# Kernel optimization log

Measured on AMD Instinct MI355X. Metric: run time of the kernel, lower is better.

The kernel has to match this reference:

```python
import jax, jax.numpy as jnp
import numpy as np

# bi-degrees (0,0),(1,0),(0,1),(1,1) -> d = (2a+1)*(2b+1)
DEG_DIMS = [1, 3, 3, 9]
P, C = 8192, 256


def setup_inputs() -> dict:
    key = jax.random.key(0)
    kx, k0, k1, k2 = jax.random.split(key, 4)
    scale = 1.0 / np.sqrt(C).astype(np.float32)
    x = jax.random.normal(kx, (P, C, sum(DEG_DIMS)), dtype=jnp.float32)
    # torch.randn(mo, mi) / sqrt(mi); W10 is shared by degrees (1,0) and (0,1)
    W00 = jax.random.normal(k0, (C, C), dtype=jnp.float32) * scale
    W10 = jax.random.normal(k1, (C, C), dtype=jnp.float32) * scale
    W11 = jax.random.normal(k2, (C, C), dtype=jnp.float32) * scale
    return {"x": x, "W00": W00, "W10": W10, "W11": W11}


def reference(x, W00, W10, W11):
    # Weight for each degree segment; (0,1) reuses W10 (parameter tying in GLinear)
    Ws = [W00, W10, W10, W11]
    offsets = np.concatenate([[0], np.cumsum(DEG_DIMS)])
    outs = []
    for W, a, b in zip(Ws, offsets[:-1], offsets[1:]):
        v = x[:, :, a:b]                      # (p, c_in, d_k)
        outs.append(jnp.einsum('oi,pid->pod', W, v))
    out = jnp.concatenate(outs, axis=-1)      # (p, c_out, sum_d)
    # use_skip with matching shared channel -> residual add of input
    return out + x
```

## Files before the change

kernel.cpp:

```cpp
#include <hip/hip_runtime.h>
#include <hip/hip_bf16.h>


#define C_DIM   256
#define D_DIM   16
#define P_TILE  16
#define KC      64
#define LDS_ROW 72
#define UNITS   4
#define NFRAG   (2 * 8 * 24 * 64)
#define WS_NEEDED (NFRAG * 16)

typedef __attribute__((ext_vector_type(8))) short  short8v;
typedef __attribute__((ext_vector_type(4))) float  float4v;
typedef __attribute__((ext_vector_type(4))) unsigned int uint4v;

__device__ __forceinline__ unsigned int pack_bf16x2_rne(float lo, float hi) {
    unsigned int ul = __builtin_bit_cast(unsigned int, lo);
    unsigned int uh = __builtin_bit_cast(unsigned int, hi);
    ul = (ul + 0x7fffu + ((ul >> 16) & 1u)) >> 16;
    uh = (uh + 0x7fffu + ((uh >> 16) & 1u));
    return (ul & 0xffffu) | (uh & 0xffff0000u);
}

__device__ __forceinline__ unsigned int pack_bf16x2_tr(float lo, float hi) {
    return __builtin_amdgcn_perm(__builtin_bit_cast(unsigned int, hi),
                                 __builtin_bit_cast(unsigned int, lo),
                                 0x07060302u);
}

__device__ __forceinline__ short8v load_w_frag(const float* __restrict__ W, int row, int col) {
    const float* p = W + (size_t)row * C_DIM + col;
    float4v a = *(const float4v*)p;
    float4v b = *(const float4v*)(p + 4);
    uint4v u;
    u.x = pack_bf16x2_tr(a.x, a.y);
    u.y = pack_bf16x2_tr(a.z, a.w);
    u.z = pack_bf16x2_tr(b.x, b.y);
    u.w = pack_bf16x2_tr(b.z, b.w);
    return __builtin_bit_cast(short8v, u);
}

__device__ __forceinline__ void glds16(const float* g, float* l) {
    __builtin_amdgcn_global_load_lds(
        (const __attribute__((address_space(1))) void*)g,
        (__attribute__((address_space(3))) void*)l,
        16, 0, 0);
}

__global__ __launch_bounds__(256, 4) void init_w_pack(
    const float* __restrict__ W00, const float* __restrict__ W10,
    const float* __restrict__ W11, uint4v* __restrict__ ws)
{
    const int tid = blockIdx.x * 256 + threadIdx.x;
    if (tid >= NFRAG) return;
    const int l   = tid & 63;
    int idx = tid >> 6;
    const int f  = idx % 24;
    idx /= 24;
    const int w  = idx & 7;
    const int oh = idx >> 3;
    const int mat = f % 3;
    const int ks  = (f / 3) & 1;
    const int ic  = f / 6;
    const float* Wm = (mat == 0) ? W00 : (mat == 1) ? W10 : W11;
    const int row = oh * 128 + w * 16 + (l & 15);
    const int col = ic * KC + ks * 32 + (l >> 4) * 8;
    const float* p = Wm + (size_t)row * C_DIM + col;
    float4v a = *(const float4v*)p;
    float4v b = *(const float4v*)(p + 4);
    uint4v u;
    u.x = pack_bf16x2_rne(a.x, a.y);
    u.y = pack_bf16x2_rne(a.z, a.w);
    u.z = pack_bf16x2_rne(b.x, b.y);
    u.w = pack_bf16x2_rne(b.z, b.w);
    ws[tid] = u;
}

__global__ __launch_bounds__(512, 2) void glinear_kernel(
    const float* __restrict__ x, const float* __restrict__ W00,
    const float* __restrict__ W10, const float* __restrict__ W11,
    float* __restrict__ out, const short8v* __restrict__ wpack, int use_ws)
{
    __shared__ __align__(16) float f32s[64 * 256];
    __shared__ __align__(16) unsigned short ls[2][P_TILE * D_DIM * LDS_ROW];

    const int t    = threadIdx.x;
    const int lane = t & 63;
    const int w    = t >> 6;
    const int lm   = lane & 15;
    const int quad = lane >> 4;

    const int oh    = blockIdx.x & 1;
    const int pg    = blockIdx.x >> 1;
    const int obase = oh * 128 + w * 16;
    const int orow  = obase + lm;

    const int d4    = t & 3;
    const int ip    = (t >> 2) & 31;
    const int pq    = t >> 7;
    const int i_loc = ip * 2;

    short8v wf[4][2][3];
    if (use_ws && wpack != nullptr) {
        const short8v* wbase = wpack + ((size_t)(oh * 8 + w) * 24) * 64 + lane;
        #pragma unroll
        for (int ic = 0; ic < 4; ++ic)
            #pragma unroll
            for (int ks = 0; ks < 2; ++ks)
                #pragma unroll
                for (int mat = 0; mat < 3; ++mat)
                    wf[ic][ks][mat] = wbase[(size_t)(ic * 6 + ks * 3 + mat) * 64];
    } else {
        #pragma unroll
        for (int ic = 0; ic < 4; ++ic)
            #pragma unroll
            for (int ks = 0; ks < 2; ++ks) {
                const int col = ic * KC + ks * 32 + quad * 8;
                wf[ic][ks][0] = load_w_frag(W00, orow, col);
                wf[ic][ks][1] = load_w_frag(W10, orow, col);
                wf[ic][ks][2] = load_w_frag(W11, orow, col);
            }
    }
    asm volatile("" ::: "memory");

    auto stage_chunk = [&](int pb, int ic) {
        #pragma unroll
        for (int it = 0; it < 4; ++it) {
            const float* src = x + ((size_t)(pb + pq + it * 4) * C_DIM
                                    + (ic * KC + i_loc)) * D_DIM + d4 * 4;
            glds16(src,         &f32s[((it * 2 + 0) * 8 + w) << 8]);
            glds16(src + D_DIM, &f32s[((it * 2 + 1) * 8 + w) << 8]);
        }
    };

    stage_chunk(pg * UNITS * P_TILE, 0);

    for (int u = 0; u < UNITS; ++u) {
        const int pbase = (pg * UNITS + u) * P_TILE;

        float4v acc[16];
        const float4v fzero = {0.f, 0.f, 0.f, 0.f};
        #pragma unroll
        for (int b = 0; b < 16; ++b) acc[b] = fzero;

        #pragma unroll
        for (int ic = 0; ic < 4; ++ic) {
            const int ib = ic & 1;

            asm volatile("s_waitcnt vmcnt(0)" ::: "memory");

            #pragma unroll
            for (int it = 0; it < 4; ++it) {
                const int p = pq + it * 4;
                float4v a = *(const float4v*)&f32s[((((it * 2 + 0) * 8 + w) << 8)) + lane * 4];
                float4v b = *(const float4v*)&f32s[((((it * 2 + 1) * 8 + w) << 8)) + lane * 4];
                const int g = (i_loc >> 3) ^ (p & 7);
                const int e = i_loc & 7;
                const int base = (p * D_DIM + d4 * 4) * LDS_ROW + g * 8 + e;
                #pragma unroll
                for (int dj = 0; dj < 4; ++dj) {
                    *(unsigned int*)(&ls[ib][base + dj * LDS_ROW]) = pack_bf16x2_rne(a[dj], b[dj]);
                }
            }
            __syncthreads();

            if (ic < 3)               stage_chunk(pbase, ic + 1);
            else if (u < UNITS - 1)   stage_chunk(pbase + P_TILE, 0);
            asm volatile("" ::: "memory");

            #pragma unroll
            for (int ks = 0; ks < 2; ++ks) {
                const int gq = ((ks * 4 + quad) ^ (lm & 7));
                const unsigned short* brow = &ls[ib][lm * D_DIM * LDS_ROW + gq * 8];

                #pragma unroll
                for (int dd = 0; dd < 16; ++dd) {
                    short8v xf = *(const short8v*)(brow + dd * LDS_ROW);
                    short8v wv = (dd == 0) ? wf[ic][ks][0]
                               : (dd <= 6) ? wf[ic][ks][1]
                                           : wf[ic][ks][2];
                    acc[dd] = __builtin_amdgcn_mfma_f32_16x16x32_bf16(xf, wv, acc[dd], 0, 0, 0);
                }
            }
        }

        #pragma unroll
        for (int r = 0; r < 4; ++r) {
            const int p = pbase + quad * 4 + r;
            const int o = obase + lm;
            const size_t off = (size_t)p * (C_DIM * D_DIM) + (size_t)o * D_DIM;
            #pragma unroll
            for (int g = 0; g < 4; ++g) {
                float4v v;
                v.x = acc[g * 4 + 0][r];
                v.y = acc[g * 4 + 1][r];
                v.z = acc[g * 4 + 2][r];
                v.w = acc[g * 4 + 3][r];
                float4v xr = *(const float4v*)(x + off + g * 4);
                *(float4v*)(out + off + g * 4) = v + xr;
            }
        }
    }
}

extern "C" void kernel_launch(void* const* d_in, const int* in_sizes, int n_in,
                              void* d_out, int out_size, void* d_ws, size_t ws_size,
                              hipStream_t stream) {
    const float* x   = (const float*)d_in[0];
    const float* W00 = (const float*)d_in[1];
    const float* W10 = (const float*)d_in[2];
    const float* W11 = (const float*)d_in[3];
    float* out = (float*)d_out;

    const int use_ws = (d_ws != nullptr && ws_size >= WS_NEEDED) ? 1 : 0;
    if (use_ws) {
        hipLaunchKernelGGL(init_w_pack, dim3(96), dim3(256), 0, stream,
                           W00, W10, W11, (uint4v*)d_ws);
    }
    hipLaunchKernelGGL(glinear_kernel, dim3(256), dim3(512), 0, stream,
                       x, W00, W10, W11, out, (const short8v*)d_ws, use_ws);
}
```

Before: 279.5 us.

## Halve K-chunk and stream weight fragments per chunk to double occupancy

The input-channel chunk drops from 64 to 32, so the fp32 staging and bf16 LDS buffers shrink. Weight fragments are no longer all held in registers up front; each chunk's fragments are loaded just before that chunk is used. Together these cut LDS and VGPR use enough to raise launch bounds to 4 blocks per CU, and the grid grows to 512 blocks with 2 units each. The trade-off is twice as many barriers and staging rounds per tile, plus weight loads from global/L2 inside the main loop instead of once per block.

```diff
diff --git a/kernel.cpp b/kernel.cpp
--- a/kernel.cpp
+++ b/kernel.cpp
@@ -5,9 +5,10 @@
 #define C_DIM   256
 #define D_DIM   16
 #define P_TILE  16
-#define KC      64
-#define LDS_ROW 72
-#define UNITS   4
+#define KC      32
+#define NCH     8
+#define LDS_ROW 40
+#define UNITS   2
 #define NFRAG   (2 * 8 * 24 * 64)
 #define WS_NEEDED (NFRAG * 16)
 
@@ -65,7 +66,7 @@
     const int ic  = f / 6;
     const float* Wm = (mat == 0) ? W00 : (mat == 1) ? W10 : W11;
     const int row = oh * 128 + w * 16 + (l & 15);
-    const int col = ic * KC + ks * 32 + (l >> 4) * 8;
+    const int col = ic * 64 + ks * 32 + (l >> 4) * 8;
     const float* p = Wm + (size_t)row * C_DIM + col;
     float4v a = *(const float4v*)p;
     float4v b = *(const float4v*)(p + 4);
@@ -77,63 +78,54 @@
     ws[tid] = u;
 }
 
-__global__ __launch_bounds__(512, 2) void glinear_kernel(
+__global__ __launch_bounds__(512, 4) void glinear_kernel(
     const float* __restrict__ x, const float* __restrict__ W00,
     const float* __restrict__ W10, const float* __restrict__ W11,
     float* __restrict__ out, const short8v* __restrict__ wpack, int use_ws)
 {
-    __shared__ __align__(16) float f32s[64 * 256];
-    __shared__ __align__(16) unsigned short ls[2][P_TILE * D_DIM * LDS_ROW];
+    __shared__ __align__(16) float f32s[32 * 256];
+    __shared__ __align__(16) unsigned short ls[2][256 * LDS_ROW];
 
     const int t    = threadIdx.x;
     const int lane = t & 63;
     const int w    = t >> 6;
     const int lm   = lane & 15;
     const int quad = lane >> 4;
+    const int d4   = lane & 3;
+    const int ip   = (lane >> 2) & 15;
 
     const int oh    = blockIdx.x & 1;
     const int pg    = blockIdx.x >> 1;
     const int obase = oh * 128 + w * 16;
     const int orow  = obase + lm;
 
-    const int d4    = t & 3;
-    const int ip    = (t >> 2) & 31;
-    const int pq    = t >> 7;
-    const int i_loc = ip * 2;
-
-    short8v wf[4][2][3];
-    if (use_ws && wpack != nullptr) {
-        const short8v* wbase = wpack + ((size_t)(oh * 8 + w) * 24) * 64 + lane;
-        #pragma unroll
-        for (int ic = 0; ic < 4; ++ic)
-            #pragma unroll
-            for (int ks = 0; ks < 2; ++ks)
-                #pragma unroll
-                for (int mat = 0; mat < 3; ++mat)
-                    wf[ic][ks][mat] = wbase[(size_t)(ic * 6 + ks * 3 + mat) * 64];
-    } else {
-        #pragma unroll
-        for (int ic = 0; ic < 4; ++ic)
-            #pragma unroll
-            for (int ks = 0; ks < 2; ++ks) {
-                const int col = ic * KC + ks * 32 + quad * 8;
-                wf[ic][ks][0] = load_w_frag(W00, orow, col);
-                wf[ic][ks][1] = load_w_frag(W10, orow, col);
-                wf[ic][ks][2] = load_w_frag(W11, orow, col);
-            }
-    }
-    asm volatile("" ::: "memory");
-
-    auto stage_chunk = [&](int pb, int ic) {
-        #pragma unroll
-        for (int it = 0; it < 4; ++it) {
-            const float* src = x + ((size_t)(pb + pq + it * 4) * C_DIM
-                                    + (ic * KC + i_loc)) * D_DIM + d4 * 4;
-            glds16(src,         &f32s[((it * 2 + 0) * 8 + w) << 8]);
-            glds16(src + D_DIM, &f32s[((it * 2 + 1) * 8 + w) << 8]);
+    const short8v* wbase = wpack + ((size_t)(oh * 8 + w) * 24) * 64 + lane;
+
+    short8v wf[NCH][3];
+    auto loadW = [&](int c) {
+        if (use_ws) {
+            #pragma unroll
+            for (int mat = 0; mat < 3; ++mat)
+                wf[c][mat] = wbase[(size_t)((c >> 1) * 6 + (c & 1) * 3 + mat) * 64];
+        } else {
+            const int col = (c >> 1) * 64 + (c & 1) * 32 + quad * 8;
+            wf[c][0] = load_w_frag(W00, orow, col);
+            wf[c][1] = load_w_frag(W10, orow, col);
+            wf[c][2] = load_w_frag(W11, orow, col);
         }
     };
 
+    auto stage_chunk = [&](int pb, int c) {
+        #pragma unroll
+        for (int j = 0; j < 4; ++j) {
+            const int p = w + (j >> 1) * 8;
+            const int i = c * KC + ip * 2 + (j & 1);
+            const float* src = x + ((size_t)(pb + p) * C_DIM + i) * D_DIM + d4 * 4;
+            glds16(src, &f32s[(w * 4 + j) << 8]);
+        }
+    };
+
+    loadW(0);
     stage_chunk(pg * UNITS * P_TILE, 0);
 
     for (int u = 0; u < UNITS; ++u) {
@@ -145,43 +137,40 @@
         for (int b = 0; b < 16; ++b) acc[b] = fzero;
 
         #pragma unroll
-        for (int ic = 0; ic < 4; ++ic) {
-            const int ib = ic & 1;
+        for (int c = 0; c < NCH; ++c) {
+            const int ib = c & 1;
 
             asm volatile("s_waitcnt vmcnt(0)" ::: "memory");
 
             #pragma unroll
-            for (int it = 0; it < 4; ++it) {
-                const int p = pq + it * 4;
-                float4v a = *(const float4v*)&f32s[((((it * 2 + 0) * 8 + w) << 8)) + lane * 4];
-                float4v b = *(const float4v*)&f32s[((((it * 2 + 1) * 8 + w) << 8)) + lane * 4];
-                const int g = (i_loc >> 3) ^ (p & 7);
-                const int e = i_loc & 7;
-                const int base = (p * D_DIM + d4 * 4) * LDS_ROW + g * 8 + e;
+            for (int m = 0; m < 2; ++m) {
+                const int p = w + m * 8;
+                float4v a = *(const float4v*)&f32s[((w * 4 + m * 2 + 0) << 8) + lane * 4];
+                float4v b = *(const float4v*)&f32s[((w * 4 + m * 2 + 1) << 8) + lane * 4];
+                const int cb = (((ip >> 2) ^ (p & 3)) * 8 + (ip & 3) * 2);
                 #pragma unroll
                 for (int dj = 0; dj < 4; ++dj) {
-                    *(unsigned int*)(&ls[ib][base + dj * LDS_ROW]) = pack_bf16x2_rne(a[dj], b[dj]);
+                    const int row = (d4 * 4 + dj) * 16 + p;
+                    *(unsigned int*)&ls[ib][row * LDS_ROW + cb] = pack_bf16x2_rne(a[dj], b[dj]);
                 }
             }
             __syncthreads();
 
-            if (ic < 3)               stage_chunk(pbase, ic + 1);
-            else if (u < UNITS - 1)   stage_chunk(pbase + P_TILE, 0);
+            const bool last = (u == UNITS - 1) && (c == NCH - 1);
+            if (!last) {
+                const int nc = (c + 1) & (NCH - 1);
+                loadW(nc);
+                stage_chunk((c == NCH - 1) ? pbase + P_TILE : pbase, nc);
+            }
             asm volatile("" ::: "memory");
 
             #pragma unroll
-            for (int ks = 0; ks < 2; ++ks) {
-                const int gq = ((ks * 4 + quad) ^ (lm & 7));
-                const unsigned short* brow = &ls[ib][lm * D_DIM * LDS_ROW + gq * 8];
-
-                #pragma unroll
-                for (int dd = 0; dd < 16; ++dd) {
-                    short8v xf = *(const short8v*)(brow + dd * LDS_ROW);
-                    short8v wv = (dd == 0) ? wf[ic][ks][0]
-                               : (dd <= 6) ? wf[ic][ks][1]
-                                           : wf[ic][ks][2];
-                    acc[dd] = __builtin_amdgcn_mfma_f32_16x16x32_bf16(xf, wv, acc[dd], 0, 0, 0);
-                }
+            for (int dd = 0; dd < 16; ++dd) {
+                const int row = dd * 16 + lm;
+                const int gq  = quad ^ (lm & 3);
+                short8v xf = *(const short8v*)&ls[ib][row * LDS_ROW + gq * 8];
+                short8v wv = (dd == 0) ? wf[c][0] : (dd <= 6) ? wf[c][1] : wf[c][2];
+                acc[dd] = __builtin_amdgcn_mfma_f32_16x16x32_bf16(xf, wv, acc[dd], 0, 0, 0);
             }
         }
 
@@ -218,6 +207,6 @@
         hipLaunchKernelGGL(init_w_pack, dim3(96), dim3(256), 0, stream,
                            W00, W10, W11, (uint4v*)d_ws);
     }
-    hipLaunchKernelGGL(glinear_kernel, dim3(256), dim3(512), 0, stream,
+    hipLaunchKernelGGL(glinear_kernel, dim3(512), dim3(512), 0, stream,
                        x, W00, W10, W11, out, (const short8v*)d_ws, use_ws);
 }
```

Result: slower. 334.7 us (+19.7%).
